# Performance work log

Hardware: AMD Instinct MI355X
Metric: run time of the kernel (lower is better)

The kernel has to match this reference:

```python
import jax, jax.numpy as jnp
import numpy as np

N_EMBD = 1024
HEAD_SIZE = 64

def setup_inputs() -> dict:
    key = jax.random.key(0)
    kx, kk, kq, kv = jax.random.split(key, 4)
    B, T = 8, 2048
    x = jax.random.normal(kx, (B, T, N_EMBD), dtype=jnp.float32)
    s = 1.0 / np.sqrt(N_EMBD)  # torch Linear default init scale (kaiming-uniform-ish)
    Wk = jax.random.uniform(kk, (N_EMBD, HEAD_SIZE), jnp.float32, -s, s)
    Wq = jax.random.uniform(kq, (N_EMBD, HEAD_SIZE), jnp.float32, -s, s)
    Wv = jax.random.uniform(kv, (N_EMBD, HEAD_SIZE), jnp.float32, -s, s)
    return {"x": x, "Wk": Wk, "Wq": Wq, "Wv": Wv}

def reference(x, Wk, Wq, Wv):
    # x: (B,T,C); projections to (B,T,H)
    k = jnp.einsum('btc,ch->bth', x, Wk)
    q = jnp.einsum('btc,ch->bth', x, Wq)
    v = jnp.einsum('btc,ch->bth', x, Wv)
    T = x.shape[1]
    scale = k.shape[-1] ** -0.5
    wei = jnp.einsum('bth,bsh->bts', q, k) * scale  # (B,T,T)
    causal = jnp.tril(jnp.ones((T, T), dtype=bool))
    wei = jnp.where(causal, wei, -jnp.inf)
    wei = jax.nn.softmax(wei, axis=-1)
    out = jnp.einsum('bts,bsh->bth', wei, v)  # (B,T,H)
    return out
```

## Files before the change

kernel.cpp:

```cpp
#include <hip/hip_runtime.h>
#include <math.h>

namespace {
constexpr int BATCH = 8;
constexpr int TSEQ  = 2048;
constexpr int CDIM  = 1024;
constexpr int HDIM  = 64;
constexpr int MROWS = BATCH * TSEQ;
constexpr int NTILE = 128;
constexpr int NSLC  = 4;
constexpr float QSCALE = 0.125f * 1.4426950408889634f;
}

typedef __attribute__((ext_vector_type(4))) float  f32x4;
typedef __attribute__((ext_vector_type(8))) short  s16x8;
typedef __attribute__((ext_vector_type(4))) unsigned short u16x4;

__device__ __forceinline__ unsigned short f2bf(float f) {
    union { float f; unsigned u; } c{f};
    unsigned r = c.u + 0x7FFFu + ((c.u >> 16) & 1u);
    return (unsigned short)(r >> 16);
}

__global__ __launch_bounds__(256)
void wswz_kernel(const float* __restrict__ Wk, const float* __restrict__ Wq,
                 const float* __restrict__ Wv, unsigned short* __restrict__ swz)
{
    const int idx  = blockIdx.x * 256 + threadIdx.x;
    const int j    = idx & 7;
    const int lane = (idx >> 3) & 63;
    const int rest = idx >> 9;
    const int tn   = rest % 12;
    const int ksg  = rest / 12;
    const int kk   = ksg * 32 + (lane >> 4) * 8 + j;
    const int n    = tn * 16 + (lane & 15);
    float val;
    if (n < 64)       val = Wq[kk * HDIM + n] * QSCALE;
    else if (n < 128) val = Wk[kk * HDIM + (n - 64)];
    else              val = Wv[kk * HDIM + (n - 128)];
    swz[idx] = f2bf(val);
}

__global__ __launch_bounds__(512, 4)
void proj_kernel(const float* __restrict__ x, const unsigned short* __restrict__ swz,
                 unsigned short* __restrict__ q, unsigned short* __restrict__ k,
                 unsigned short* __restrict__ vt)
{
    __shared__ unsigned short xl[32][1032];

    const int tid  = threadIdx.x;
    const int lane = tid & 63, wave = tid >> 6;
    const int quad = lane >> 4, l15 = lane & 15;
    const int mh   = wave >> 2;
    const int cq   = wave & 3;
    const int m0   = blockIdx.x * 32;

    {
        const float* xb = x + (size_t)m0 * CDIM;
        float4 t[16];
        #pragma unroll
        for (int i = 0; i < 16; ++i)
            t[i] = *(const float4*)(xb + i * 2048 + tid * 4);
        #pragma unroll
        for (int i = 0; i < 16; ++i) {
            const int o = i * 2048 + tid * 4;
            u16x4 p;
            p[0] = f2bf(t[i].x); p[1] = f2bf(t[i].y);
            p[2] = f2bf(t[i].z); p[3] = f2bf(t[i].w);
            *(u16x4*)&xl[o >> 10][o & 1023] = p;
        }
    }
    __syncthreads();

    f32x4 acc[3] = {};
    const unsigned short* bp = swz + ((size_t)(cq * 3) * 64 + lane) * 8;
    s16x8 b0 = *(const s16x8*)(bp);
    s16x8 b1 = *(const s16x8*)(bp + 512);
    s16x8 b2 = *(const s16x8*)(bp + 1024);
    bp += 6144;

    #pragma unroll
    for (int ks = 0; ks < 32; ++ks) {
        s16x8 nb0, nb1, nb2;
        if (ks < 31) {
            nb0 = *(const s16x8*)(bp);
            nb1 = *(const s16x8*)(bp + 512);
            nb2 = *(const s16x8*)(bp + 1024);
            bp += 6144;
        }
        const s16x8 af = *(const s16x8*)&xl[mh * 16 + l15][ks * 32 + quad * 8];
        acc[0] = __builtin_amdgcn_mfma_f32_16x16x32_bf16(af, b0, acc[0], 0, 0, 0);
        acc[1] = __builtin_amdgcn_mfma_f32_16x16x32_bf16(af, b1, acc[1], 0, 0, 0);
        acc[2] = __builtin_amdgcn_mfma_f32_16x16x32_bf16(af, b2, acc[2], 0, 0, 0);
        if (ks < 31) { b0 = nb0; b1 = nb1; b2 = nb2; }
    }

    const int rowg = m0 + mh * 16 + quad * 4;
    #pragma unroll
    for (int t = 0; t < 3; ++t) {
        const int n = cq * 48 + t * 16 + l15;
        if (n < 64) {
            #pragma unroll
            for (int r = 0; r < 4; ++r)
                q[(size_t)(rowg + r) * HDIM + n] = f2bf(acc[t][r]);
        } else if (n < 128) {
            #pragma unroll
            for (int r = 0; r < 4; ++r)
                k[(size_t)(rowg + r) * HDIM + (n - 64)] = f2bf(acc[t][r]);
        } else {
            const int h  = n - 128;
            const int bb = rowg >> 11, tl = rowg & 2047;
            u16x4 pv;
            #pragma unroll
            for (int r = 0; r < 4; ++r) pv[r] = f2bf(acc[t][r]);
            *(u16x4*)(vt + ((size_t)bb * HDIM + h) * TSEQ + tl) = pv;
        }
    }
}

__global__ __launch_bounds__(256, 4)
void attn_part(const unsigned short* __restrict__ q, const unsigned short* __restrict__ k,
               const unsigned short* __restrict__ vt, float* __restrict__ Opart,
               float* __restrict__ lpart)
{
    __shared__ unsigned short Pl[4][16][72];
    __shared__ float Olds[4][16][68];
    __shared__ float llds[4][16];

    const int tid  = threadIdx.x;
    const int lane = tid & 63, wave = tid >> 6;
    const int quad = lane >> 4, l15 = lane & 15;
    const int b    = blockIdx.y;
    const int s    = blockIdx.x & 3;
    const int ti   = 127 - ((int)blockIdx.x >> 2);
    const int m0   = ti * 16;
    const int nt   = ti / 4 + 1;

    const unsigned short* qb  = q  + (size_t)b * TSEQ * HDIM;
    const unsigned short* kb  = k  + (size_t)b * TSEQ * HDIM;
    const unsigned short* vtb = vt + (size_t)b * HDIM * TSEQ;

    s16x8 aq[2];
    #pragma unroll
    for (int ks = 0; ks < 2; ++ks)
        aq[ks] = *(const s16x8*)(qb + (size_t)(m0 + l15) * HDIM + ks * 32 + quad * 8);

    f32x4 O[4] = {};
    float l_lane[4] = {0.f, 0.f, 0.f, 0.f};

    for (int c = s + 4 * wave; c < nt; c += 16) {
        const int n0 = c * 64;

        f32x4 S[4] = {};
        #pragma unroll
        for (int st = 0; st < 4; ++st) {
            const unsigned short* kr = kb + (size_t)(n0 + st * 16 + l15) * HDIM + quad * 8;
            const s16x8 k0 = *(const s16x8*)(kr);
            const s16x8 k1 = *(const s16x8*)(kr + 32);
            S[st] = __builtin_amdgcn_mfma_f32_16x16x32_bf16(aq[0], k0, S[st], 0, 0, 0);
            S[st] = __builtin_amdgcn_mfma_f32_16x16x32_bf16(aq[1], k1, S[st], 0, 0, 0);
        }

        const int rowbase = m0 + quad * 4;
        #pragma unroll
        for (int st = 0; st < 4; ++st) {
            const int col = n0 + st * 16 + l15;
            #pragma unroll
            for (int r = 0; r < 4; ++r) {
                const float p = (col > rowbase + r) ? 0.f : exp2f(S[st][r]);
                S[st][r] = p;
                l_lane[r] += p;
            }
        }

        #pragma unroll
        for (int st = 0; st < 4; ++st)
            #pragma unroll
            for (int r = 0; r < 4; ++r)
                Pl[wave][quad * 4 + r][st * 16 + l15] = f2bf(S[st][r]);
        s16x8 pa[2];
        #pragma unroll
        for (int ks = 0; ks < 2; ++ks)
            pa[ks] = *(const s16x8*)&Pl[wave][l15][ks * 32 + quad * 8];

        #pragma unroll
        for (int hst = 0; hst < 4; ++hst) {
            const unsigned short* vr = vtb + (size_t)(hst * 16 + l15) * TSEQ + n0 + quad * 8;
            const s16x8 v0 = *(const s16x8*)(vr);
            const s16x8 v1 = *(const s16x8*)(vr + 32);
            O[hst] = __builtin_amdgcn_mfma_f32_16x16x32_bf16(pa[0], v0, O[hst], 0, 0, 0);
            O[hst] = __builtin_amdgcn_mfma_f32_16x16x32_bf16(pa[1], v1, O[hst], 0, 0, 0);
        }
    }

    #pragma unroll
    for (int off = 1; off < 16; off <<= 1)
        #pragma unroll
        for (int r = 0; r < 4; ++r)
            l_lane[r] += __shfl_xor(l_lane[r], off);

    #pragma unroll
    for (int hst = 0; hst < 4; ++hst)
        #pragma unroll
        for (int r = 0; r < 4; ++r)
            Olds[wave][quad * 4 + r][hst * 16 + l15] = O[hst][r];
    if (l15 == 0) {
        #pragma unroll
        for (int r = 0; r < 4; ++r)
            llds[wave][quad * 4 + r] = l_lane[r];
    }
    __syncthreads();

    const size_t p = ((size_t)b * NTILE + ti) * NSLC + s;
    {
        const int r  = tid >> 4;
        const int c4 = (tid & 15) << 2;
        float4 t;
        float* tp = &t.x;
        #pragma unroll
        for (int j = 0; j < 4; ++j)
            tp[j] = Olds[0][r][c4 + j] + Olds[1][r][c4 + j] +
                    Olds[2][r][c4 + j] + Olds[3][r][c4 + j];
        *(float4*)(Opart + (p * 16 + r) * HDIM + c4) = t;
        if ((tid & 15) == 0)
            lpart[p * 16 + r] = llds[0][r] + llds[1][r] + llds[2][r] + llds[3][r];
    }
}

__global__ __launch_bounds__(256)
void attn_combine(const float* __restrict__ Opart, const float* __restrict__ lpart,
                  float* __restrict__ out)
{
    const int g   = blockIdx.x * 256 + threadIdx.x;
    const int row = g >> 4;
    const int c4  = (g & 15) << 2;
    const int b   = row >> 11, t = row & 2047;
    const int ti  = t >> 4,  r = t & 15;
    const size_t p0 = ((size_t)b * NTILE + ti) * NSLC;

    float4 acc = {0.f, 0.f, 0.f, 0.f};
    float lv = 0.f;
    #pragma unroll
    for (int s = 0; s < NSLC; ++s) {
        const float4 t4 = *(const float4*)(Opart + ((p0 + s) * 16 + r) * HDIM + c4);
        acc.x += t4.x; acc.y += t4.y; acc.z += t4.z; acc.w += t4.w;
        lv += lpart[(p0 + s) * 16 + r];
    }
    const float inv = 1.f / lv;
    float4 o = {acc.x * inv, acc.y * inv, acc.z * inv, acc.w * inv};
    *(float4*)(out + (size_t)row * HDIM + c4) = o;
}

extern "C" void kernel_launch(void* const* d_in, const int* in_sizes, int n_in,
                              void* d_out, int out_size, void* d_ws, size_t ws_size,
                              hipStream_t stream) {
    const float* x  = (const float*)d_in[0];
    const float* Wk = (const float*)d_in[1];
    const float* Wq = (const float*)d_in[2];
    const float* Wv = (const float*)d_in[3];
    float* out = (float*)d_out;

    unsigned short* swz = (unsigned short*)d_ws;
    unsigned short* qw  = swz + 196608;
    unsigned short* kw  = qw + (size_t)MROWS * HDIM;
    unsigned short* vtw = kw + (size_t)MROWS * HDIM;
    float* Opart = (float*)(vtw + (size_t)MROWS * HDIM);
    float* lpart = Opart + (size_t)BATCH * NTILE * NSLC * 16 * HDIM;

    wswz_kernel<<<dim3(768), 256, 0, stream>>>(Wk, Wq, Wv, swz);
    proj_kernel<<<dim3(MROWS / 32), 512, 0, stream>>>(x, swz, qw, kw, vtw);
    attn_part<<<dim3(NTILE * NSLC, BATCH), 256, 0, stream>>>(qw, kw, vtw, Opart, lpart);
    attn_combine<<<dim3(MROWS * 16 / 256), 256, 0, stream>>>(Opart, lpart, out);
}
```

Before: 157.7 us.

## Assign key-splits to waves within one block and prefetch V fragments

Each attention block now handles one query tile. Its four waves act as the four key-range splits, so the grid shrinks from 4096 to 1024 blocks. Each wave writes its own partial output and row sum straight to global memory, which removes the LDS reduction and the block barrier. V fragments are also loaded at the top of each chunk iteration so their latency overlaps the QK MFMAs and softmax. In exchange there are fewer blocks to hide latency, causal work is less balanced across waves, and the partial stores are scalar and less coalesced.

Result: slower. 175.4 us (+11.2%).

```diff
diff --git a/kernel.cpp b/kernel.cpp
--- a/kernel.cpp
+++ b/kernel.cpp
@@ -124,15 +124,13 @@
                float* __restrict__ lpart)
 {
     __shared__ unsigned short Pl[4][16][72];
-    __shared__ float Olds[4][16][68];
-    __shared__ float llds[4][16];
 
     const int tid  = threadIdx.x;
     const int lane = tid & 63, wave = tid >> 6;
     const int quad = lane >> 4, l15 = lane & 15;
     const int b    = blockIdx.y;
-    const int s    = blockIdx.x & 3;
-    const int ti   = 127 - ((int)blockIdx.x >> 2);
+    const int s    = wave;
+    const int ti   = 127 - (int)blockIdx.x;
     const int m0   = ti * 16;
     const int nt   = ti / 4 + 1;
 
@@ -148,8 +146,16 @@
     f32x4 O[4] = {};
     float l_lane[4] = {0.f, 0.f, 0.f, 0.f};
 
-    for (int c = s + 4 * wave; c < nt; c += 16) {
+    for (int c = s; c < nt; c += 4) {
         const int n0 = c * 64;
+
+        s16x8 vf[4][2];
+        #pragma unroll
+        for (int hst = 0; hst < 4; ++hst) {
+            const unsigned short* vr = vtb + (size_t)(hst * 16 + l15) * TSEQ + n0 + quad * 8;
+            vf[hst][0] = *(const s16x8*)(vr);
+            vf[hst][1] = *(const s16x8*)(vr + 32);
+        }
 
         f32x4 S[4] = {};
         #pragma unroll
@@ -185,11 +191,8 @@
 
         #pragma unroll
         for (int hst = 0; hst < 4; ++hst) {
-            const unsigned short* vr = vtb + (size_t)(hst * 16 + l15) * TSEQ + n0 + quad * 8;
-            const s16x8 v0 = *(const s16x8*)(vr);
-            const s16x8 v1 = *(const s16x8*)(vr + 32);
-            O[hst] = __builtin_amdgcn_mfma_f32_16x16x32_bf16(pa[0], v0, O[hst], 0, 0, 0);
-            O[hst] = __builtin_amdgcn_mfma_f32_16x16x32_bf16(pa[1], v1, O[hst], 0, 0, 0);
+            O[hst] = __builtin_amdgcn_mfma_f32_16x16x32_bf16(pa[0], vf[hst][0], O[hst], 0, 0, 0);
+            O[hst] = __builtin_amdgcn_mfma_f32_16x16x32_bf16(pa[1], vf[hst][1], O[hst], 0, 0, 0);
         }
     }
 
@@ -199,31 +202,16 @@
         for (int r = 0; r < 4; ++r)
             l_lane[r] += __shfl_xor(l_lane[r], off);
 
+    const size_t p = ((size_t)b * NTILE + ti) * NSLC + s;
     #pragma unroll
     for (int hst = 0; hst < 4; ++hst)
         #pragma unroll
         for (int r = 0; r < 4; ++r)
-            Olds[wave][quad * 4 + r][hst * 16 + l15] = O[hst][r];
+            Opart[(p * 16 + quad * 4 + r) * HDIM + hst * 16 + l15] = O[hst][r];
     if (l15 == 0) {
         #pragma unroll
         for (int r = 0; r < 4; ++r)
-            llds[wave][quad * 4 + r] = l_lane[r];
-    }
-    __syncthreads();
-
-    const size_t p = ((size_t)b * NTILE + ti) * NSLC + s;
-    {
-        const int r  = tid >> 4;
-        const int c4 = (tid & 15) << 2;
-        float4 t;
-        float* tp = &t.x;
-        #pragma unroll
-        for (int j = 0; j < 4; ++j)
-            tp[j] = Olds[0][r][c4 + j] + Olds[1][r][c4 + j] +
-                    Olds[2][r][c4 + j] + Olds[3][r][c4 + j];
-        *(float4*)(Opart + (p * 16 + r) * HDIM + c4) = t;
-        if ((tid & 15) == 0)
-            lpart[p * 16 + r] = llds[0][r] + llds[1][r] + llds[2][r] + llds[3][r];
+            lpart[p * 16 + quad * 4 + r] = l_lane[r];
     }
 }
 
@@ -269,6 +257,6 @@
 
     wswz_kernel<<<dim3(768), 256, 0, stream>>>(Wk, Wq, Wv, swz);
     proj_kernel<<<dim3(MROWS / 32), 512, 0, stream>>>(x, swz, qw, kw, vtw);
-    attn_part<<<dim3(NTILE * NSLC, BATCH), 256, 0, stream>>>(qw, kw, vtw, Opart, lpart);
+    attn_part<<<dim3(NTILE, BATCH), 256, 0, stream>>>(qw, kw, vtw, Opart, lpart);
     attn_combine<<<dim3(MROWS * 16 / 256), 256, 0, stream>>>(Opart, lpart, out);
 }
```
